# Kernel optimization log

Hardware: AMD Instinct MI355X
Metric: run time of the kernel (lower is better)

Reference implementation:

```python
import jax, jax.numpy as jnp
import numpy as np

B, T, N, F_IN = 32, 64, 128, 16
H, SOUT = 64, 16
D = N * SOUT            # transformer d_model = 2048
NHEADS, DH = 16, 128
DFF, LAYERS = 2048, 2
NCLASSES, OUT = 8, 10
THR = 0.004             # edge threshold on sigmoid(V)/N


def setup_inputs():
    key = jax.random.key(0)
    ks = iter(jax.random.split(key, 40))
    r = lambda *s: jax.random.normal(next(ks), s, jnp.float32) * 0.02
    return {
        'X': jax.random.normal(next(ks), (B, T, N * F_IN), jnp.float32),
        'V_Adap': jax.random.normal(next(ks), (NCLASSES, N, N), jnp.float32),
        'Wl': r(F_IN, H), 'bl': jnp.zeros((H,)),
        'Wr': r(F_IN, H), 'br': jnp.zeros((H,)),
        'att': jax.random.normal(next(ks), (H,), jnp.float32) * 0.1,
        'gat_bias': jnp.zeros((H,)),
        'Wfc': r(H, SOUT), 'bfc': jnp.zeros((SOUT,)),
        'Wq': r(LAYERS, D, D), 'bq': jnp.zeros((LAYERS, D)),
        'Wk': r(LAYERS, D, D), 'bk': jnp.zeros((LAYERS, D)),
        'Wv': r(LAYERS, D, D), 'bv': jnp.zeros((LAYERS, D)),
        'Wo': r(LAYERS, D, D), 'bo': jnp.zeros((LAYERS, D)),
        'ln1_g': jnp.ones((LAYERS, D)), 'ln1_b': jnp.zeros((LAYERS, D)),
        'W1': r(LAYERS, D, DFF), 'b1': jnp.zeros((LAYERS, DFF)),
        'W2': r(LAYERS, DFF, D), 'b2': jnp.zeros((LAYERS, D)),
        'ln2_g': jnp.ones((LAYERS, D)), 'ln2_b': jnp.zeros((LAYERS, D)),
        'Wout': r(D, OUT), 'bout': jnp.zeros((OUT,)),
        'class_idx': 2,
    }


def _ln(x, g, b):
    mu = jnp.mean(x, -1, keepdims=True)
    var = jnp.var(x, -1, keepdims=True)
    return (x - mu) / jnp.sqrt(var + 1e-5) * g + b


def reference(X, V_Adap, Wl, bl, Wr, br, att, gat_bias, Wfc, bfc,
              Wq, bq, Wk, bk, Wv, bv, Wo, bo, ln1_g, ln1_b,
              W1, b1, W2, b2, ln2_g, ln2_b, Wout, bout, class_idx):
    # dynamic adjacency: sigmoid + scale + threshold (data-dependent sparsity as a mask)
    A = jax.nn.sigmoid(V_Adap[class_idx]) / N
    mask = (A > THR) | jnp.eye(N, dtype=bool)   # GATv2Conv default add_self_loops

    def gat_step(x_t):                           # x_t: (B, N, F_IN)
        xl = x_t @ Wl + bl                       # source transform (B, N, H)
        xr = x_t @ Wr + br                       # target transform (B, N, H)
        s = jax.nn.leaky_relu(xl[:, :, None, :] + xr[:, None, :, :], 0.2)  # (B, src, dst, H)
        e = jnp.where(mask[None], jnp.einsum('bijh,h->bij', s, att), -1e9)
        alpha = jax.nn.softmax(e, axis=1)        # softmax over sources per target node
        out = jnp.einsum('bij,bih->bjh', alpha, xl) + gat_bias
        return out @ Wfc + bfc                   # (B, N, SOUT)

    Xr = X.reshape(B, T, N, F_IN).transpose(1, 0, 2, 3)   # (T, B, N, F)
    spatial = jax.lax.map(gat_step, Xr)                   # (T, B, N, SOUT)
    h = spatial.transpose(1, 0, 2, 3).reshape(B, T, D)

    # post-norm TransformerEncoder (torch defaults: relu, d_ff=2048, no dropout at eval)
    for l in range(LAYERS):
        q = (h @ Wq[l] + bq[l]).reshape(B, T, NHEADS, DH).transpose(0, 2, 1, 3)
        k = (h @ Wk[l] + bk[l]).reshape(B, T, NHEADS, DH).transpose(0, 2, 1, 3)
        v = (h @ Wv[l] + bv[l]).reshape(B, T, NHEADS, DH).transpose(0, 2, 1, 3)
        aw = jax.nn.softmax(jnp.einsum('bhqd,bhkd->bhqk', q, k) / np.float32(np.sqrt(DH)), axis=-1)
        ao = jnp.einsum('bhqk,bhkd->bhqd', aw, v).transpose(0, 2, 1, 3).reshape(B, T, D)
        h = _ln(h + ao @ Wo[l] + bo[l], ln1_g[l], ln1_b[l])
        ff = jax.nn.relu(h @ W1[l] + b1[l]) @ W2[l] + b2[l]
        h = _ln(h + ff, ln2_g[l], ln2_b[l])

    return h[:, -1, :] @ Wout + bout             # (B, OUT)
```

## Files before the change

### kernel.cpp

```cpp
#include <hip/hip_runtime.h>
#include <cstdint>
#include <cstddef>


typedef unsigned short u16;
typedef __bf16 bf16x8 __attribute__((ext_vector_type(8)));
typedef float f32x4 __attribute__((ext_vector_type(4)));
typedef float f32x2 __attribute__((ext_vector_type(2)));
typedef unsigned int u32x4 __attribute__((ext_vector_type(4)));
typedef float f32x4v __attribute__((ext_vector_type(4)));
typedef unsigned short u16x4 __attribute__((ext_vector_type(4)));

__device__ __forceinline__ u16 f2b(float f) {
  union { float f; unsigned u; } x; x.f = f;
  unsigned r = x.u + 0x7fffu + ((x.u >> 16) & 1u);
  return (u16)(r >> 16);
}
__device__ __forceinline__ float b2f(u16 s) {
  union { unsigned u; float f; } x; x.u = ((unsigned)s) << 16;
  return x.f;
}
__device__ __forceinline__ float b2f_lo(unsigned q) {
  union { unsigned u; float f; } x; x.u = q << 16;
  return x.f;
}
__device__ __forceinline__ float b2f_hi(unsigned q) {
  union { unsigned u; float f; } x; x.u = q & 0xffff0000u;
  return x.f;
}

__device__ __forceinline__ void gload_lds16(const void* g, void* l) {
  __builtin_amdgcn_global_load_lds(
      (const __attribute__((address_space(1))) unsigned int*)g,
      (__attribute__((address_space(3))) unsigned int*)l, 16, 0, 0);
}

__global__ __launch_bounds__(1024) void gat_kernel(
    const float* __restrict__ X, const float* __restrict__ V_Adap,
    const int* __restrict__ class_idx,
    const float* __restrict__ Wl, const float* __restrict__ bl,
    const float* __restrict__ Wr, const float* __restrict__ br,
    const float* __restrict__ att, const float* __restrict__ gat_bias,
    const float* __restrict__ Wfc, const float* __restrict__ bfc,
    float* __restrict__ h_f32, u16* __restrict__ h_b16)
{
  const int bt = blockIdx.x;
  const int tid = threadIdx.x;

  __shared__ __align__(16) float xlT[64 * 132];
  __shared__ __align__(16) float xrT[64 * 132];
  __shared__ __align__(16) u16   xlTb[64 * 136];
  __shared__ __align__(16) u16   esbT[128 * 136];
  __shared__ __align__(16) u16   aggb[128 * 72];
  __shared__ __align__(16) float WlT[64 * 20];
  __shared__ __align__(16) float WrT[64 * 20];
  __shared__ __align__(16) float WfcT[16 * 66];
  __shared__ float atts[64], bls[64], brs[64], gbias[64], bfcs[16];
  __shared__ float cls[128], crs[128], inv_s[128];
  __shared__ float red[8 * 128];

  float* scratchX = (float*)aggb;

  {
    const int h = tid >> 4, f = tid & 15;
    WlT[h * 20 + f] = Wl[f * 64 + h];
    WrT[h * 20 + f] = Wr[f * 64 + h];
    WfcT[f * 66 + h] = Wfc[h * 16 + f];
  }
  if (tid < 64) { atts[tid] = att[tid]; bls[tid] = bl[tid]; brs[tid] = br[tid]; gbias[tid] = gat_bias[tid]; }
  if (tid < 16) bfcs[tid] = bfc[tid];
  if (tid < 512)
    ((f32x4*)scratchX)[tid] = ((const f32x4*)(X + (size_t)bt * 2048))[tid];
  const int cidx = *class_idx;
  __syncthreads();

  {
    const int h = tid & 63, ng = tid >> 6;
    f32x4 wl4[4], wr4[4];
    #pragma unroll
    for (int f4 = 0; f4 < 4; f4++) {
      wl4[f4] = *(const f32x4*)&WlT[h * 20 + f4 * 4];
      wr4[f4] = *(const f32x4*)&WrT[h * 20 + f4 * 4];
    }
    const float blh = bls[h], brh = brs[h];
    float al8[8], ar8[8];
    #pragma unroll
    for (int t = 0; t < 8; t++) {
      const int n = ng * 8 + t;
      float al = blh, ar = brh;
      #pragma unroll
      for (int f4 = 0; f4 < 4; f4++) {
        const f32x4 xv = *(const f32x4*)&scratchX[n * 16 + f4 * 4];
        #pragma unroll
        for (int f = 0; f < 4; f++) {
          al = fmaf(xv[f], wl4[f4][f], al);
          ar = fmaf(xv[f], wr4[f4][f], ar);
        }
      }
      al8[t] = al; ar8[t] = ar;
    }
    *(f32x4*)&xlT[h * 132 + ng * 8]     = *(f32x4*)&al8[0];
    *(f32x4*)&xlT[h * 132 + ng * 8 + 4] = *(f32x4*)&al8[4];
    *(f32x4*)&xrT[h * 132 + ng * 8]     = *(f32x4*)&ar8[0];
    *(f32x4*)&xrT[h * 132 + ng * 8 + 4] = *(f32x4*)&ar8[4];
    u16 pb[8];
    #pragma unroll
    for (int t = 0; t < 8; t++) pb[t] = f2b(al8[t]);
    *(u16x4*)&xlTb[h * 136 + ng * 8]     = *(u16x4*)&pb[0];
    *(u16x4*)&xlTb[h * 136 + ng * 8 + 4] = *(u16x4*)&pb[4];
  }
  __syncthreads();

  {
    const int n = tid & 127, g = tid >> 7;
    const float* srcT = (g < 4) ? xlT : xrT;
    const int h0 = (g & 3) * 16;
    float s = 0.f;
    #pragma unroll
    for (int hh = 0; hh < 16; hh++)
      s = fmaf(atts[h0 + hh], srcT[(h0 + hh) * 132 + n], s);
    red[g * 128 + n] = s;
  }
  __syncthreads();
  if (tid < 256) {
    const int n = tid & 127;
    const int base = (tid < 128) ? 0 : 4;
    const float s = ((red[base * 128 + n] + red[(base + 1) * 128 + n])
                   + red[(base + 2) * 128 + n]) + red[(base + 3) * 128 + n];
    if (tid < 128) cls[n] = s; else crs[n] = s;
  }
  __syncthreads();

  {
    const int i0 = (tid >> 6) * 8;
    const int j0 = (tid & 63) * 2;
    float acc[8][2] = {};
    #pragma unroll 8
    for (int h = 0; h < 64; h++) {
      const float ah = att[h];
      const f32x4 xa0 = *(const f32x4*)&xlT[h * 132 + i0];
      const f32x4 xa1 = *(const f32x4*)&xlT[h * 132 + i0 + 4];
      const f32x2 xb  = *(const f32x2*)&xrT[h * 132 + j0];
      #pragma unroll
      for (int a = 0; a < 4; a++) {
        acc[a][0]     = fmaf(ah, __builtin_fabsf(xa0[a] + xb[0]), acc[a][0]);
        acc[a][1]     = fmaf(ah, __builtin_fabsf(xa0[a] + xb[1]), acc[a][1]);
        acc[4 + a][0] = fmaf(ah, __builtin_fabsf(xa1[a] + xb[0]), acc[4 + a][0]);
        acc[4 + a][1] = fmaf(ah, __builtin_fabsf(xa1[a] + xb[1]), acc[4 + a][1]);
      }
    }
    const float* Vc = V_Adap + (size_t)cidx * 16384;
    float vm[8][2];
    #pragma unroll
    for (int a = 0; a < 8; a++) {
      const f32x2 vc = *(const f32x2*)&Vc[(size_t)(i0 + a) * 128 + j0];
      vm[a][0] = vc[0]; vm[a][1] = vc[1];
    }
    const f32x4 cl0 = *(const f32x4*)&cls[i0];
    const f32x4 cl1 = *(const f32x4*)&cls[i0 + 4];
    float cli[8] = {cl0[0], cl0[1], cl0[2], cl0[3], cl1[0], cl1[1], cl1[2], cl1[3]};
    #pragma unroll
    for (int b = 0; b < 2; b++) {
      const int j = j0 + b;
      const float ej = 0.6f * crs[j];
      u16 pk[8];
      #pragma unroll
      for (int a = 0; a < 8; a++) {
        const int i = i0 + a;
        const float e = ej + 0.6f * cli[a] + 0.4f * acc[a][b];
        const bool m = (vm[a][b] > 0.04800922f) || (i == j);
        pk[a] = f2b(m ? e : -1e9f);
      }
      *(u16x4*)&esbT[j * 136 + i0]     = *(u16x4*)&pk[0];
      *(u16x4*)&esbT[j * 136 + i0 + 4] = *(u16x4*)&pk[4];
    }
  }
  __syncthreads();

  {
    const int j = tid >> 3, c = tid & 7;
    u16* rp = &esbT[j * 136 + c * 16];
    float ps = 0.f;
    #pragma unroll
    for (int half = 0; half < 2; half++) {
      u32x4 q = *(u32x4*)(rp + half * 8);
      #pragma unroll
      for (int w2 = 0; w2 < 4; w2++) {
        const float p0 = __expf(b2f_lo(q[w2]));
        const float p1 = __expf(b2f_hi(q[w2]));
        ps += p0 + p1;
        q[w2] = (unsigned)f2b(p0) | ((unsigned)f2b(p1) << 16);
      }
      *(u32x4*)(rp + half * 8) = q;
    }
    red[c * 128 + j] = ps;
  }
  __syncthreads();
  if (tid < 128) {
    float s = 0.f;
    #pragma unroll
    for (int c = 0; c < 8; c++) s += red[c * 128 + tid];
    inv_s[tid] = 1.f / s;
  }
  __syncthreads();

  {
    const int w = tid >> 6, lane = tid & 63;
    const int lq = lane >> 4, lr = lane & 15;
    const int jt = w >> 1, ht0 = (w & 1) * 2;
    f32x4 acc2[2] = {};
    #pragma unroll
    for (int ks = 0; ks < 4; ks++) {
      const bf16x8 af = __builtin_bit_cast(bf16x8,
          *(const u32x4*)&esbT[(jt * 16 + lr) * 136 + ks * 32 + lq * 8]);
      #pragma unroll
      for (int t = 0; t < 2; t++) {
        const bf16x8 bfb = __builtin_bit_cast(bf16x8,
            *(const u32x4*)&xlTb[((ht0 + t) * 16 + lr) * 136 + ks * 32 + lq * 8]);
        acc2[t] = __builtin_amdgcn_mfma_f32_16x16x32_bf16(af, bfb, acc2[t], 0, 0, 0);
      }
    }
    #pragma unroll
    for (int t = 0; t < 2; t++) {
      const int h = (ht0 + t) * 16 + lr;
      const float gb = gbias[h];
      #pragma unroll
      for (int r = 0; r < 4; r++) {
        const int j = jt * 16 + lq * 4 + r;
        aggb[j * 72 + h] = f2b(acc2[t][r] * inv_s[j] + gb);
      }
    }
  }
  __syncthreads();

  {
    const int j = tid >> 3, s0 = (tid & 7) * 2;
    float o0 = bfcs[s0], o1 = bfcs[s0 + 1];
    #pragma unroll
    for (int h8 = 0; h8 < 8; h8++) {
      u32x4 q = *(const u32x4*)&aggb[j * 72 + h8 * 8];
      #pragma unroll
      for (int w2 = 0; w2 < 4; w2++) {
        const int h = h8 * 8 + w2 * 2;
        const float a0 = b2f_lo(q[w2]);
        const float a1 = b2f_hi(q[w2]);
        o0 = fmaf(a0, WfcT[s0 * 66 + h], o0);
        o1 = fmaf(a0, WfcT[(s0 + 1) * 66 + h], o1);
        o0 = fmaf(a1, WfcT[s0 * 66 + h + 1], o0);
        o1 = fmaf(a1, WfcT[(s0 + 1) * 66 + h + 1], o1);
      }
    }
    const size_t off = (size_t)bt * 2048 + j * 16 + s0;
    h_f32[off] = o0; h_f32[off + 1] = o1;
    h_b16[off] = f2b(o0); h_b16[off + 1] = f2b(o1);
  }
}

struct TransArgs {
  const float* s0; const float* s1; const float* s2;
  u16* d0; u16* d1; u16* d2;
};

__global__ __launch_bounds__(256) void transpose_cast(TransArgs p)
{
  const float* src = (blockIdx.z == 0) ? p.s0 : (blockIdx.z == 1) ? p.s1 : p.s2;
  u16* dst = (blockIdx.z == 0) ? p.d0 : (blockIdx.z == 1) ? p.d1 : p.d2;
  __shared__ u16 tile[64][66];
  const int k0 = blockIdx.y * 64, n0 = blockIdx.x * 64;
  const int tid = threadIdx.x;
  const int c = tid & 63, rb = tid >> 6;
  #pragma unroll
  for (int r = 0; r < 16; r++) {
    const int k = rb + r * 4;
    tile[k][c] = f2b(src[(size_t)(k0 + k) * 2048 + n0 + c]);
  }
  __syncthreads();
  #pragma unroll
  for (int r = 0; r < 16; r++) {
    const int n = rb + r * 4;
    dst[(size_t)(n0 + n) * 2048 + k0 + c] = tile[c][n];
  }
}

struct GemmArgs {
  const u16* A;
  const u16* Bt0; const u16* Bt1; const u16* Bt2;
  const float* b0; const float* b1; const float* b2;
  void* C0; void* C1; void* C2;
  int N; int K;
};

template <int MODE>
__global__ __launch_bounds__(256) void gemm_bt(GemmArgs g)
{
  const int z = blockIdx.z;
  const u16* Bt = (z == 0) ? g.Bt0 : (z == 1) ? g.Bt1 : g.Bt2;
  const float* bias = (z == 0) ? g.b0 : (z == 1) ? g.b1 : g.b2;
  void* C = (z == 0) ? g.C0 : (z == 1) ? g.C1 : g.C2;
  const int N = g.N, K = g.K;
  const int m0 = blockIdx.y * 128, n0 = blockIdx.x * 128;

  __shared__ __align__(16) u16 As[2][128 * 32];
  __shared__ __align__(16) u16 Bs[2][128 * 32];

  const int tid = threadIdx.x;
  const int lane = tid & 63, w = tid >> 6;
  const int srow = w * 16 + (lane >> 2);
  const int scol = ((lane & 3) ^ ((lane >> 2) & 3)) * 8;
  const u16* gA = g.A + (size_t)(m0 + srow) * K + scol;
  const u16* gB = Bt + (size_t)(n0 + srow) * K + scol;
  const int lbase = (w * 16) * 32;

  const int wm = (w >> 1) * 64, wn = (w & 1) * 64;
  const int lq = lane >> 4, lr = lane & 15;
  const int csw = (lr & 3) << 3;

  f32x4 acc[4][4] = {};
  const int NT = K >> 5;

  auto stage = [&](int buf, int kt) {
    const int kk = kt << 5;
    #pragma unroll
    for (int c = 0; c < 2; c++) {
      gload_lds16(gA + (size_t)(c * 64) * K + kk, &As[buf][lbase + c * 64 * 32]);
      gload_lds16(gB + (size_t)(c * 64) * K + kk, &Bs[buf][lbase + c * 64 * 32]);
    }
  };
  auto compute = [&](int buf) {
    bf16x8 af[4], bfr[4];
    #pragma unroll
    for (int i = 0; i < 4; i++) {
      af[i] = __builtin_bit_cast(bf16x8,
          *(const u32x4*)&As[buf][(wm + i * 16 + lr) * 32 + ((lq * 8) ^ csw)]);
      bfr[i] = __builtin_bit_cast(bf16x8,
          *(const u32x4*)&Bs[buf][(wn + i * 16 + lr) * 32 + ((lq * 8) ^ csw)]);
    }
    #pragma unroll
    for (int mi = 0; mi < 4; mi++)
      #pragma unroll
      for (int ni = 0; ni < 4; ni++)
        acc[mi][ni] = __builtin_amdgcn_mfma_f32_16x16x32_bf16(af[mi], bfr[ni], acc[mi][ni], 0, 0, 0);
  };

  stage(0, 0);
  __syncthreads();
  int cur = 0;
  for (int kt = 0; kt + 1 < NT; ++kt) {
    stage(cur ^ 1, kt + 1);
    compute(cur);
    __syncthreads();
    cur ^= 1;
  }
  compute(cur);

  #pragma unroll
  for (int ni = 0; ni < 4; ni++) {
    const int col = n0 + wn + ni * 16 + lr;
    const float bv = bias[col];
    #pragma unroll
    for (int mi = 0; mi < 4; mi++) {
      #pragma unroll
      for (int r = 0; r < 4; r++) {
        const int row = m0 + wm + mi * 16 + lq * 4 + r;
        float v = acc[mi][ni][r] + bv;
        if (MODE == 0) {
          ((float*)C)[(size_t)row * N + col] = v;
        } else {
          if (MODE == 2) v = fmaxf(v, 0.f);
          ((u16*)C)[(size_t)row * N + col] = f2b(v);
        }
      }
    }
  }
}

template <int MODE>
__global__ __launch_bounds__(256) void gemm_bt64(GemmArgs g)
{
  const u16* Bt = g.Bt0;
  const float* bias = g.b0;
  void* C = g.C0;
  const int N = g.N, K = g.K;
  const int m0 = blockIdx.y * 128, n0 = blockIdx.x * 64;

  __shared__ __align__(16) u16 As[2][128 * 64];
  __shared__ __align__(16) u16 Bs[2][64 * 64];

  const int tid = threadIdx.x;
  const int lane = tid & 63, w = tid >> 6;
  const int srow = w * 8 + (lane >> 3);
  const int scol = ((lane & 7) ^ (lane >> 3)) * 8;
  const u16* gA = g.A + (size_t)(m0 + srow) * K + scol;
  const u16* gB = Bt + (size_t)(n0 + srow) * K + scol;
  const int lbase = (w * 8) * 64;

  const int wm = w * 32;
  const int lq = lane >> 4, lr = lane & 15;
  const int csw = (lr & 7) << 3;

  f32x4 acc[2][4] = {};
  const int NT = K >> 6;

  auto stage = [&](int buf, int kt) {
    const int kk = kt << 6;
    #pragma unroll
    for (int c = 0; c < 4; c++)
      gload_lds16(gA + (size_t)(c * 32) * K + kk, &As[buf][lbase + c * 32 * 64]);
    #pragma unroll
    for (int c = 0; c < 2; c++)
      gload_lds16(gB + (size_t)(c * 32) * K + kk, &Bs[buf][lbase + c * 32 * 64]);
  };
  auto compute = [&](int buf) {
    #pragma unroll
    for (int ks = 0; ks < 2; ks++) {
      bf16x8 af[2], bfr[4];
      #pragma unroll
      for (int i = 0; i < 2; i++)
        af[i] = __builtin_bit_cast(bf16x8,
            *(const u32x4*)&As[buf][(wm + i * 16 + lr) * 64 + ((ks * 32 + lq * 8) ^ csw)]);
      #pragma unroll
      for (int i = 0; i < 4; i++)
        bfr[i] = __builtin_bit_cast(bf16x8,
            *(const u32x4*)&Bs[buf][(i * 16 + lr) * 64 + ((ks * 32 + lq * 8) ^ csw)]);
      #pragma unroll
      for (int mi = 0; mi < 2; mi++)
        #pragma unroll
        for (int ni = 0; ni < 4; ni++)
          acc[mi][ni] = __builtin_amdgcn_mfma_f32_16x16x32_bf16(af[mi], bfr[ni], acc[mi][ni], 0, 0, 0);
    }
  };

  stage(0, 0);
  __syncthreads();
  int cur = 0;
  for (int kt = 0; kt + 1 < NT; ++kt) {
    stage(cur ^ 1, kt + 1);
    compute(cur);
    __syncthreads();
    cur ^= 1;
  }
  compute(cur);

  #pragma unroll
  for (int ni = 0; ni < 4; ni++) {
    const int col = n0 + ni * 16 + lr;
    const float bv = bias[col];
    #pragma unroll
    for (int mi = 0; mi < 2; mi++) {
      #pragma unroll
      for (int r = 0; r < 4; r++) {
        const int row = m0 + wm + mi * 16 + lq * 4 + r;
        float v = acc[mi][ni][r] + bv;
        if (MODE == 0) {
          ((float*)C)[(size_t)row * N + col] = v;
        } else {
          if (MODE == 2) v = fmaxf(v, 0.f);
          ((u16*)C)[(size_t)row * N + col] = f2b(v);
        }
      }
    }
  }
}

__global__ __launch_bounds__(256) void attn_kernel(
    const u16* __restrict__ Qb, const u16* __restrict__ Kb,
    const u16* __restrict__ Vb, u16* __restrict__ AOb)
{
  const int head = blockIdx.x, b = blockIdx.y;
  const int tid = threadIdx.x;
  __shared__ __align__(16) float qs[64 * 132];
  __shared__ __align__(16) float ks[64 * 132];
  __shared__ __align__(16) float vs[64 * 128];
  __shared__ __align__(16) float ss[64 * 65];
  const size_t base = ((size_t)b * 64) * 2048 + (size_t)head * 128;

  for (int idx = tid; idx < 1024; idx += 256) {
    const int t_ = idx >> 4, d8 = (idx & 15) * 8;
    const size_t gp = base + (size_t)t_ * 2048 + d8;
    const u32x4 q = *(const u32x4*)(Qb + gp);
    const u32x4 k = *(const u32x4*)(Kb + gp);
    const u32x4 v = *(const u32x4*)(Vb + gp);
    f32x4 q0 = {b2f_lo(q[0]), b2f_hi(q[0]), b2f_lo(q[1]), b2f_hi(q[1])};
    f32x4 q1 = {b2f_lo(q[2]), b2f_hi(q[2]), b2f_lo(q[3]), b2f_hi(q[3])};
    f32x4 k0 = {b2f_lo(k[0]), b2f_hi(k[0]), b2f_lo(k[1]), b2f_hi(k[1])};
    f32x4 k1 = {b2f_lo(k[2]), b2f_hi(k[2]), b2f_lo(k[3]), b2f_hi(k[3])};
    f32x4 v0 = {b2f_lo(v[0]), b2f_hi(v[0]), b2f_lo(v[1]), b2f_hi(v[1])};
    f32x4 v1 = {b2f_lo(v[2]), b2f_hi(v[2]), b2f_lo(v[3]), b2f_hi(v[3])};
    *(f32x4*)&qs[t_ * 132 + d8] = q0; *(f32x4*)&qs[t_ * 132 + d8 + 4] = q1;
    *(f32x4*)&ks[t_ * 132 + d8] = k0; *(f32x4*)&ks[t_ * 132 + d8 + 4] = k1;
    *(f32x4*)&vs[t_ * 128 + d8] = v0; *(f32x4*)&vs[t_ * 128 + d8 + 4] = v1;
  }
  __syncthreads();

  {
    const int i0 = (tid >> 4) * 4, j0 = tid & 15;
    float acc[4][4] = {};
    #pragma unroll 2
    for (int d0 = 0; d0 < 128; d0 += 4) {
      f32x4 qv[4], kv[4];
      #pragma unroll
      for (int a = 0; a < 4; a++) qv[a] = *(const f32x4*)&qs[(i0 + a) * 132 + d0];
      #pragma unroll
      for (int c = 0; c < 4; c++) kv[c] = *(const f32x4*)&ks[(j0 + c * 16) * 132 + d0];
      #pragma unroll
      for (int a = 0; a < 4; a++)
        #pragma unroll
        for (int c = 0; c < 4; c++)
          #pragma unroll
          for (int e = 0; e < 4; e++)
            acc[a][c] = fmaf(qv[a][e], kv[c][e], acc[a][c]);
    }
    const float sc = 0.08838834764831845f;
    #pragma unroll
    for (int a = 0; a < 4; a++)
      #pragma unroll
      for (int c = 0; c < 4; c++)
        ss[(i0 + a) * 65 + j0 + c * 16] = acc[a][c] * sc;
  }
  __syncthreads();

  {
    const int row = tid >> 2;
    float* rp = &ss[row * 65 + (tid & 3) * 16];
    float mx = -3e38f;
    #pragma unroll
    for (int j = 0; j < 16; j++) mx = fmaxf(mx, rp[j]);
    mx = fmaxf(mx, __shfl_xor(mx, 1, 64));
    mx = fmaxf(mx, __shfl_xor(mx, 2, 64));
    float s = 0.f;
    #pragma unroll
    for (int j = 0; j < 16; j++) { const float p = __expf(rp[j] - mx); rp[j] = p; s += p; }
    s += __shfl_xor(s, 1, 64);
    s += __shfl_xor(s, 2, 64);
    const float inv = 1.f / s;
    #pragma unroll
    for (int j = 0; j < 16; j++) rp[j] *= inv;
  }
  __syncthreads();

  {
    const int i0 = (tid >> 4) * 4, d0 = (tid & 15) * 8;
    float o[4][8] = {};
    for (int j = 0; j < 64; j++) {
      float pv[4];
      #pragma unroll
      for (int a = 0; a < 4; a++) pv[a] = ss[(i0 + a) * 65 + j];
      f32x4v v0 = *(const f32x4v*)&vs[j * 128 + d0];
      f32x4v v1 = *(const f32x4v*)&vs[j * 128 + d0 + 4];
      float vv[8] = {v0[0], v0[1], v0[2], v0[3], v1[0], v1[1], v1[2], v1[3]};
      #pragma unroll
      for (int a = 0; a < 4; a++)
        #pragma unroll
        for (int c = 0; c < 8; c++)
          o[a][c] = fmaf(pv[a], vv[c], o[a][c]);
    }
    #pragma unroll
    for (int a = 0; a < 4; a++)
      #pragma unroll
      for (int c = 0; c < 8; c++)
        AOb[base + (size_t)(i0 + a) * 2048 + d0 + c] = f2b(o[a][c]);
  }
}

__global__ __launch_bounds__(256) void ln_kernel(
    const float* __restrict__ hin, const float* __restrict__ delta,
    const float* __restrict__ gamma, const float* __restrict__ beta,
    float* __restrict__ hout, u16* __restrict__ bout_)
{
  const int token = blockIdx.x, tid = threadIdx.x;
  const size_t off = (size_t)token * 2048;
  __shared__ float red[8];
  f32x4 v[2];
  float s = 0.f;
  #pragma unroll
  for (int r = 0; r < 2; r++) {
    const int i = r * 1024 + tid * 4;
    const f32x4 a = *(const f32x4*)(hin + off + i);
    const f32x4 b = *(const f32x4*)(delta + off + i);
    v[r] = a + b;
    s += v[r][0] + v[r][1] + v[r][2] + v[r][3];
  }
  #pragma unroll
  for (int o = 32; o > 0; o >>= 1) s += __shfl_down(s, o, 64);
  if ((tid & 63) == 0) red[tid >> 6] = s;
  __syncthreads();
  const float mean = (red[0] + red[1] + red[2] + red[3]) * (1.f / 2048.f);
  float s2 = 0.f;
  #pragma unroll
  for (int r = 0; r < 2; r++)
    #pragma unroll
    for (int e = 0; e < 4; e++) { const float d = v[r][e] - mean; s2 = fmaf(d, d, s2); }
  #pragma unroll
  for (int o = 32; o > 0; o >>= 1) s2 += __shfl_down(s2, o, 64);
  if ((tid & 63) == 0) red[4 + (tid >> 6)] = s2;
  __syncthreads();
  const float var = (red[4] + red[5] + red[6] + red[7]) * (1.f / 2048.f);
  const float rstd = rsqrtf(var + 1e-5f);
  #pragma unroll
  for (int r = 0; r < 2; r++) {
    const int i = r * 1024 + tid * 4;
    const f32x4 gm = *(const f32x4*)(gamma + i);
    const f32x4 bt = *(const f32x4*)(beta + i);
    f32x4 y;
    u16x4 pb;
    #pragma unroll
    for (int e = 0; e < 4; e++) {
      y[e] = (v[r][e] - mean) * rstd * gm[e] + bt[e];
      pb[e] = f2b(y[e]);
    }
    *(f32x4*)(hout + off + i) = y;
    *(u16x4*)(bout_ + off + i) = pb;
  }
}

__global__ __launch_bounds__(256) void final_kernel(
    const float* __restrict__ h, const float* __restrict__ Wout,
    const float* __restrict__ bout, float* __restrict__ out)
{
  const int b = blockIdx.x, tid = threadIdx.x;
  __shared__ float row[2048];
  __shared__ float part[256];
  const float* hr = h + ((size_t)b * 64 + 63) * 2048;
  for (int i = tid; i < 2048; i += 256) row[i] = hr[i];
  __syncthreads();
  const int o = tid & 15, ch = tid >> 4;
  float s = 0.f;
  if (o < 10) {
    const int i0 = ch * 128;
    for (int i = i0; i < i0 + 128; i++) s = fmaf(row[i], Wout[(size_t)i * 10 + o], s);
  }
  part[tid] = s;
  __syncthreads();
  if (tid < 10) {
    float t = bout[tid];
    for (int c2 = 0; c2 < 16; c2++) t += part[c2 * 16 + tid];
    out[(size_t)b * 10 + tid] = t;
  }
}

extern "C" void kernel_launch(void* const* d_in, const int* in_sizes, int n_in,
                              void* d_out, int out_size, void* d_ws, size_t ws_size,
                              hipStream_t stream)
{
  const float* X        = (const float*)d_in[0];
  const float* V_Adap   = (const float*)d_in[1];
  const float* Wl       = (const float*)d_in[2];
  const float* bl       = (const float*)d_in[3];
  const float* Wr       = (const float*)d_in[4];
  const float* br       = (const float*)d_in[5];
  const float* att      = (const float*)d_in[6];
  const float* gat_bias = (const float*)d_in[7];
  const float* Wfc      = (const float*)d_in[8];
  const float* bfc      = (const float*)d_in[9];
  const float* Wq       = (const float*)d_in[10];
  const float* bq       = (const float*)d_in[11];
  const float* Wk       = (const float*)d_in[12];
  const float* bk       = (const float*)d_in[13];
  const float* Wv       = (const float*)d_in[14];
  const float* bv       = (const float*)d_in[15];
  const float* Wo       = (const float*)d_in[16];
  const float* bo       = (const float*)d_in[17];
  const float* ln1_g    = (const float*)d_in[18];
  const float* ln1_b    = (const float*)d_in[19];
  const float* W1       = (const float*)d_in[20];
  const float* b1       = (const float*)d_in[21];
  const float* W2       = (const float*)d_in[22];
  const float* b2       = (const float*)d_in[23];
  const float* ln2_g    = (const float*)d_in[24];
  const float* ln2_b    = (const float*)d_in[25];
  const float* WoutP    = (const float*)d_in[26];
  const float* boutP    = (const float*)d_in[27];
  const int*   class_idx = (const int*)d_in[28];

  char* ws = (char*)d_ws;
  const size_t MB = (size_t)1 << 20;
  float* h_f32 = (float*)(ws);
  u16*   h_b16 = (u16*)(ws + 16 * MB);
  u16*   Qb    = (u16*)(ws + 24 * MB);
  u16*   Kb    = (u16*)(ws + 32 * MB);
  u16*   Vb    = (u16*)(ws + 40 * MB);
  u16*   AOb   = (u16*)(ws + 48 * MB);
  float* tmp   = (float*)(ws + 56 * MB);
  u16*   ff1b  = (u16*)(ws + 72 * MB);
  u16*   Wt0   = (u16*)(ws + 80 * MB);
  u16*   Wt1   = (u16*)(ws + 88 * MB);
  u16*   Wt2   = (u16*)(ws + 96 * MB);

  gat_kernel<<<2048, 1024, 0, stream>>>(X, V_Adap, class_idx, Wl, bl, Wr, br,
                                        att, gat_bias, Wfc, bfc, h_f32, h_b16);

  const size_t DD = 2048ull * 2048ull;
  for (int l = 0; l < 2; l++) {
    const size_t wofs = (size_t)l * DD;
    const size_t bofs = (size_t)l * 2048;

    transpose_cast<<<dim3(32, 32, 3), 256, 0, stream>>>(
        TransArgs{Wq + wofs, Wk + wofs, Wv + wofs, Wt0, Wt1, Wt2});
    gemm_bt<1><<<dim3(16, 16, 3), 256, 0, stream>>>(
        GemmArgs{h_b16, Wt0, Wt1, Wt2, bq + bofs, bk + bofs, bv + bofs,
                 Qb, Kb, Vb, 2048, 2048});

    attn_kernel<<<dim3(16, 32), 256, 0, stream>>>(Qb, Kb, Vb, AOb);

    transpose_cast<<<dim3(32, 32, 3), 256, 0, stream>>>(
        TransArgs{Wo + wofs, W1 + wofs, W2 + wofs, Wt0, Wt1, Wt2});

    gemm_bt64<0><<<dim3(32, 16), 256, 0, stream>>>(
        GemmArgs{AOb, Wt0, nullptr, nullptr, bo + bofs, nullptr, nullptr,
                 tmp, nullptr, nullptr, 2048, 2048});
    ln_kernel<<<2048, 256, 0, stream>>>(h_f32, tmp, ln1_g + bofs, ln1_b + bofs,
                                        h_f32, h_b16);

    gemm_bt64<2><<<dim3(32, 16), 256, 0, stream>>>(
        GemmArgs{h_b16, Wt1, nullptr, nullptr, b1 + bofs, nullptr, nullptr,
                 ff1b, nullptr, nullptr, 2048, 2048});

    gemm_bt64<0><<<dim3(32, 16), 256, 0, stream>>>(
        GemmArgs{ff1b, Wt2, nullptr, nullptr, b2 + bofs, nullptr, nullptr,
                 tmp, nullptr, nullptr, 2048, 2048});
    ln_kernel<<<2048, 256, 0, stream>>>(h_f32, tmp, ln2_g + bofs, ln2_b + bofs,
                                        h_f32, h_b16);
  }

  final_kernel<<<32, 256, 0, stream>>>(h_f32, WoutP, boutP, (float*)d_out);
}
```

Measured before the change: 891.0 us.

## Triple-buffer GEMM LDS staging with explicit vmcnt waits and MFMA priority

Both bf16 GEMM kernels move from double to triple LDS buffering, issuing global loads two k-tiles ahead. Each tile is gated by a partial s_waitcnt vmcnt plus raw s_barrier instead of a full __syncthreads. The compute phase raises wave priority with s_setprio. This keeps more loads in flight and hides global latency, at the cost of 50% more LDS per block (possibly lower occupancy). The vmcnt counts are hardcoded to the assumed load count per stage, so it breaks if the stage code changes.

```diff
diff --git a/kernel.cpp b/kernel.cpp
--- a/kernel.cpp
+++ b/kernel.cpp
@@ -300,8 +300,8 @@
   const int N = g.N, K = g.K;
   const int m0 = blockIdx.y * 128, n0 = blockIdx.x * 128;
 
-  __shared__ __align__(16) u16 As[2][128 * 32];
-  __shared__ __align__(16) u16 Bs[2][128 * 32];
+  __shared__ __align__(16) u16 As[3][128 * 32];
+  __shared__ __align__(16) u16 Bs[3][128 * 32];
 
   const int tid = threadIdx.x;
   const int lane = tid & 63, w = tid >> 6;
@@ -343,15 +343,28 @@
   };
 
   stage(0, 0);
-  __syncthreads();
-  int cur = 0;
-  for (int kt = 0; kt + 1 < NT; ++kt) {
-    stage(cur ^ 1, kt + 1);
-    compute(cur);
-    __syncthreads();
-    cur ^= 1;
-  }
-  compute(cur);
+  stage(1, 1);
+  int cA = 0;
+  for (int kt = 0; kt < NT; ++kt) {
+    if (kt + 2 < NT) {
+      int b2 = cA + 2; if (b2 >= 3) b2 -= 3;
+      stage(b2, kt + 2);
+      asm volatile("s_waitcnt vmcnt(8)" ::: "memory");
+    } else if (kt + 1 < NT) {
+      asm volatile("s_waitcnt vmcnt(4)" ::: "memory");
+    } else {
+      asm volatile("s_waitcnt vmcnt(0)" ::: "memory");
+    }
+    __builtin_amdgcn_s_barrier();
+    asm volatile("" ::: "memory");
+    __builtin_amdgcn_s_setprio(1);
+    compute(cA);
+    __builtin_amdgcn_s_setprio(0);
+    asm volatile("" ::: "memory");
+    __builtin_amdgcn_s_barrier();
+    asm volatile("" ::: "memory");
+    if (++cA == 3) cA = 0;
+  }
 
   #pragma unroll
   for (int ni = 0; ni < 4; ni++) {
@@ -383,8 +396,8 @@
   const int N = g.N, K = g.K;
   const int m0 = blockIdx.y * 128, n0 = blockIdx.x * 64;
 
-  __shared__ __align__(16) u16 As[2][128 * 64];
-  __shared__ __align__(16) u16 Bs[2][64 * 64];
+  __shared__ __align__(16) u16 As[3][128 * 64];
+  __shared__ __align__(16) u16 Bs[3][64 * 64];
 
   const int tid = threadIdx.x;
   const int lane = tid & 63, w = tid >> 6;
@@ -431,15 +444,28 @@
   };
 
   stage(0, 0);
-  __syncthreads();
-  int cur = 0;
-  for (int kt = 0; kt + 1 < NT; ++kt) {
-    stage(cur ^ 1, kt + 1);
-    compute(cur);
-    __syncthreads();
-    cur ^= 1;
-  }
-  compute(cur);
+  stage(1, 1);
+  int cA = 0;
+  for (int kt = 0; kt < NT; ++kt) {
+    if (kt + 2 < NT) {
+      int b2 = cA + 2; if (b2 >= 3) b2 -= 3;
+      stage(b2, kt + 2);
+      asm volatile("s_waitcnt vmcnt(12)" ::: "memory");
+    } else if (kt + 1 < NT) {
+      asm volatile("s_waitcnt vmcnt(6)" ::: "memory");
+    } else {
+      asm volatile("s_waitcnt vmcnt(0)" ::: "memory");
+    }
+    __builtin_amdgcn_s_barrier();
+    asm volatile("" ::: "memory");
+    __builtin_amdgcn_s_setprio(1);
+    compute(cA);
+    __builtin_amdgcn_s_setprio(0);
+    asm volatile("" ::: "memory");
+    __builtin_amdgcn_s_barrier();
+    asm volatile("" ::: "memory");
+    if (++cA == 3) cA = 0;
+  }
 
   #pragma unroll
   for (int ni = 0; ni < 4; ni++) {
```

After: 874.4 us. About the same (-1.9%).
